# Kernel optimization log

Measured on AMD Instinct MI355X. Metric: run time of the kernel, lower is better.

The kernel has to match this reference:

```python
import jax, jax.numpy as jnp
import numpy as np

B, S, D, H, E, K = 4, 2048, 1024, 2048, 8, 2


def setup_inputs() -> dict:
    key = jax.random.key(0)
    ks = jax.random.split(key, 5)
    x = jax.random.normal(ks[0], (B, S, D), dtype=jnp.float32)
    Wr = jax.random.normal(ks[1], (D, E), dtype=jnp.float32) * 0.02  # router weight
    w1 = jax.random.normal(ks[2], (E, D, H), dtype=jnp.float32) * 0.02  # gate proj per expert
    w3 = jax.random.normal(ks[3], (E, D, H), dtype=jnp.float32) * 0.02  # up proj per expert
    w2 = jax.random.normal(ks[4], (E, H, D), dtype=jnp.float32) * 0.02  # down proj per expert
    return {"x": x, "Wr": Wr, "w1": w1, "w2": w2, "w3": w3}


def reference(x, Wr, w1, w2, w3):
    b, s, d = x.shape
    e = Wr.shape[1]
    flat = x.reshape(b * s, d)                      # [T, D]
    logits = flat @ Wr                              # [T, E]
    probs = jax.nn.softmax(logits, axis=-1)
    vals, idx = jax.lax.top_k(probs, K)             # [T, K]
    weights = vals / jnp.sum(vals, axis=-1, keepdims=True)
    onehot = jax.nn.one_hot(idx, e, dtype=flat.dtype)   # [T, K, E]
    cw = jnp.einsum('tke,tk->te', onehot, weights)      # combine weight per (token, expert)

    # naive dense: every expert computes every token, masked by combine weights
    out = jnp.zeros_like(flat)
    for ei in range(e):  # fixed small structural loop over experts
        h = jax.nn.silu(flat @ w1[ei]) * (flat @ w3[ei])   # [T, H]
        out = out + (h @ w2[ei]) * cw[:, ei:ei + 1]

    # aux load-balancing loss (usage uses any() over top-k slots, as in torch code)
    usage = (onehot.sum(axis=1) > 0).astype(flat.dtype).mean(axis=0)  # [E]
    prob_mass = probs.mean(axis=0)                                     # [E]
    aux_loss = e * jnp.sum(usage * prob_mass)
    return out.reshape(b, s, d), aux_loss
```

## Files before the change

kernel.cpp:

```cpp
#include <hip/hip_runtime.h>
#include <hip/hip_bf16.h>
#include <cstdint>
#include <cstddef>

#define T_TOK 8192
#define DIM   1024
#define HID   2048
#define NE    8
#define CAP   2816

typedef __attribute__((ext_vector_type(8))) short bf16x8;
typedef __attribute__((ext_vector_type(4))) float f32x4;
using bf16 = __hip_bfloat16;

__device__ __forceinline__ void gload16(const bf16* g, bf16* l) {
    __builtin_amdgcn_global_load_lds(
        (const __attribute__((address_space(1))) unsigned int*)(g),
        (__attribute__((address_space(3))) unsigned int*)(l), 16, 0, 0);
}
__device__ __forceinline__ float b2f(unsigned short u) {
    return __uint_as_float(((unsigned int)u) << 16);
}
#define MFMA16(a, b, c) __builtin_amdgcn_mfma_f32_16x16x32_bf16((a), (b), (c), 0, 0, 0)

__global__ __launch_bounds__(256) void k_transpose_all(const float* __restrict__ w1,
                                                       const float* __restrict__ w3,
                                                       const float* __restrict__ w2,
                                                       bf16* __restrict__ w1t,
                                                       bf16* __restrict__ w3t,
                                                       bf16* __restrict__ w2t) {
    __shared__ float tile[64][65];
    int z = blockIdx.z;
    const float* in = (z == 0) ? w1 : (z == 1) ? w3 : w2;
    bf16* out = (z == 0) ? w1t : (z == 1) ? w3t : w2t;
    int R = (z == 2) ? HID : DIM;
    int C = (z == 2) ? DIM : HID;
    int e = blockIdx.y;
    int ct = C >> 6;
    int r0 = (blockIdx.x / ct) << 6;
    int c0 = (blockIdx.x % ct) << 6;
    const float* src = in + (size_t)e * R * C;
    bf16* dst = out + (size_t)e * R * C;
    int s = threadIdx.x & 15, g = threadIdx.x >> 4;
#pragma unroll
    for (int j = 0; j < 4; ++j) {
        int row = j * 16 + g;
        float4 v = *(const float4*)(src + (size_t)(r0 + row) * C + c0 + s * 4);
        tile[row][s * 4 + 0] = v.x; tile[row][s * 4 + 1] = v.y;
        tile[row][s * 4 + 2] = v.z; tile[row][s * 4 + 3] = v.w;
    }
    __syncthreads();
#pragma unroll
    for (int j = 0; j < 4; ++j) {
        int c = j * 16 + g;
        int r = s * 4;
        bf16 o[4] = {__float2bfloat16(tile[r][c]),     __float2bfloat16(tile[r + 1][c]),
                     __float2bfloat16(tile[r + 2][c]), __float2bfloat16(tile[r + 3][c])};
        *(uint2*)(dst + (size_t)(c0 + c) * R + r0 + r) = *(const uint2*)o;
    }
}

__global__ __launch_bounds__(256) void k_logits(const float* __restrict__ x,
                                                const float* __restrict__ Wr,
                                                float* __restrict__ logits,
                                                bf16* __restrict__ xb) {
    __shared__ float wl[NE][DIM];
    for (int o = threadIdx.x; o < NE * DIM; o += 256) {
        int e = o >> 10, d = o & (DIM - 1);
        wl[e][d] = Wr[d * NE + e];
    }
    __syncthreads();
    int wid = threadIdx.x >> 6, lane = threadIdx.x & 63;
    int t = blockIdx.x * 4 + wid;
    const float* xr = x + (size_t)t * DIM;
    double acc[NE];
#pragma unroll
    for (int e = 0; e < NE; ++e) acc[e] = 0.0;
#pragma unroll
    for (int i = 0; i < DIM / 256; ++i) {
        int base = i * 256 + lane * 4;
        float4 v = *(const float4*)(xr + base);
        bf16 o[4] = {__float2bfloat16(v.x), __float2bfloat16(v.y),
                     __float2bfloat16(v.z), __float2bfloat16(v.w)};
        *(uint2*)(xb + (size_t)t * DIM + base) = *(const uint2*)o;
#pragma unroll
        for (int e = 0; e < NE; ++e)
            acc[e] += (double)v.x * wl[e][base] + (double)v.y * wl[e][base + 1]
                    + (double)v.z * wl[e][base + 2] + (double)v.w * wl[e][base + 3];
    }
#pragma unroll
    for (int e = 0; e < NE; ++e) {
        double v = acc[e];
        for (int m = 32; m >= 1; m >>= 1) v += __shfl_xor(v, m);
        if (lane == 0) logits[t * NE + e] = (float)v;
    }
}

__global__ __launch_bounds__(256) void k_route(const float* __restrict__ logits,
                                               int* counts, int* seg_tok, float* seg_w,
                                               int* slotpos, float* probsum) {
    int t = blockIdx.x * 256 + threadIdx.x;
    float l[NE];
#pragma unroll
    for (int e = 0; e < NE; ++e) l[e] = logits[t * NE + e];
    float mx = l[0];
#pragma unroll
    for (int e = 1; e < NE; ++e) mx = fmaxf(mx, l[e]);
    float p[NE], s = 0.f;
#pragma unroll
    for (int e = 0; e < NE; ++e) { p[e] = expf(l[e] - mx); s += p[e]; }
    float inv = 1.f / s;
#pragma unroll
    for (int e = 0; e < NE; ++e) p[e] *= inv;
    int e0 = 0; float v0 = p[0];
#pragma unroll
    for (int e = 1; e < NE; ++e) if (p[e] > v0) { v0 = p[e]; e0 = e; }
    int e1 = -1; float v1 = -1.f;
#pragma unroll
    for (int e = 0; e < NE; ++e) if (e != e0 && p[e] > v1) { v1 = p[e]; e1 = e; }
    float wsum = v0 + v1;
    float w0 = v0 / wsum, w1 = v1 / wsum;

    int lane = threadIdx.x & 63, wid = threadIdx.x >> 6;
    __shared__ float ps[4][NE];
#pragma unroll
    for (int e = 0; e < NE; ++e) {
        float v = p[e];
        for (int m = 32; m >= 1; m >>= 1) v += __shfl_xor(v, m);
        if (lane == 0) ps[wid][e] = v;
    }
    __syncthreads();
    if (threadIdx.x < NE) {
        float v = ps[0][threadIdx.x] + ps[1][threadIdx.x] + ps[2][threadIdx.x] + ps[3][threadIdx.x];
        atomicAdd(&probsum[threadIdx.x], v);
    }
    for (int slot = 0; slot < 2; ++slot) {
        int   e  = slot ? e1 : e0;
        float wv = slot ? w1 : w0;
#pragma unroll
        for (int ex = 0; ex < NE; ++ex) {
            unsigned long long m = __ballot(e == ex);
            if (e == ex) {
                int leader = __ffsll(m) - 1;
                int base = 0;
                if (lane == leader) base = atomicAdd(&counts[ex], __popcll(m));
                base = __shfl(base, leader);
                int pos = base + (int)__popcll(m & ((1ull << lane) - 1ull));
                if (pos < CAP) {
                    seg_tok[ex * CAP + pos] = t;
                    seg_w[ex * CAP + pos]  = wv;
                    slotpos[2 * t + slot]  = ex * CAP + pos;
                } else {
                    slotpos[2 * t + slot]  = -1;
                }
            }
        }
    }
}

__global__ __launch_bounds__(256, 3) void k_gemm1(const bf16* __restrict__ xb,
                                                  const bf16* __restrict__ w1t,
                                                  const bf16* __restrict__ w3t,
                                                  const int* __restrict__ counts,
                                                  const int* __restrict__ seg_tok,
                                                  bf16* __restrict__ h) {
    __shared__ __align__(16) bf16 lds[16384];
    __shared__ int toks[128];
    const int NTL = HID / 64;
    int flat = blockIdx.y * gridDim.x + blockIdx.x;
    int cpx  = (gridDim.x * NE) >> 3;
    int swz  = (flat & 7) * cpx + (flat >> 3);
    int e    = swz / gridDim.x;
    int tile = swz % gridDim.x;
    int mtile = tile / NTL, ntile = tile % NTL;
    int cnt = counts[e]; if (cnt > CAP) cnt = CAP;
    if (mtile * 128 >= cnt) return;

    int tx = threadIdx.x, lane = tx & 63, w = tx >> 6;
    if (tx < 128) {
        int slot = mtile * 128 + tx;
        toks[tx] = seg_tok[e * CAP + (slot < cnt ? slot : 0)];
    }
    __syncthreads();

    int l8 = lane >> 3;
    int sch = (((lane & 7) ^ l8) << 3);
    const bf16* sA[4];
#pragma unroll
    for (int i = 0; i < 4; ++i)
        sA[i] = xb + (size_t)toks[w * 32 + i * 8 + l8] * DIM + sch;
    const bf16* sBg[2];
    const bf16* sBu[2];
#pragma unroll
    for (int j = 0; j < 2; ++j) {
        int br = ntile * 64 + w * 16 + j * 8 + l8;
        sBg[j] = w1t + ((size_t)e * HID + br) * DIM + sch;
        sBu[j] = w3t + ((size_t)e * HID + br) * DIM + sch;
    }
    bf16* dA  = lds + w * 2048 + (lane << 3);
    bf16* dBg = lds + 8192  + w * 1024 + (lane << 3);
    bf16* dBu = lds + 12288 + w * 1024 + (lane << 3);

    int l15 = lane & 15, lh = lane >> 4;
    int wm = w >> 1, wn = w & 1;
    f32x4 accg[4][2], accu[4][2];
    f32x4 zero4 = {0.f, 0.f, 0.f, 0.f};
#pragma unroll
    for (int m = 0; m < 4; ++m)
#pragma unroll
        for (int n = 0; n < 2; ++n) { accg[m][n] = zero4; accu[m][n] = zero4; }

    const int NT = DIM / 64;
#pragma unroll 1
    for (int k = 0; k < NT; ++k) {
        int ko = k * 64;
#pragma unroll
        for (int i = 0; i < 4; ++i) gload16(sA[i] + ko, dA + i * 512);
#pragma unroll
        for (int j = 0; j < 2; ++j) {
            gload16(sBg[j] + ko, dBg + j * 512);
            gload16(sBu[j] + ko, dBu + j * 512);
        }
        __syncthreads();
#pragma unroll
        for (int ks = 0; ks < 2; ++ks) {
            int co = ((((ks << 2) | lh) ^ (l15 & 7)) << 3);
            bf16x8 af[4], bg[2], bu[2];
#pragma unroll
            for (int m = 0; m < 4; ++m) {
                int row = wm * 64 + m * 16 + l15;
                af[m] = *(const bf16x8*)(lds + row * 64 + co);
            }
#pragma unroll
            for (int n = 0; n < 2; ++n) {
                int br = wn * 32 + n * 16 + l15;
                bg[n] = *(const bf16x8*)(lds + 8192 + br * 64 + co);
                bu[n] = *(const bf16x8*)(lds + 12288 + br * 64 + co);
            }
#pragma unroll
            for (int n = 0; n < 2; ++n)
#pragma unroll
                for (int m = 0; m < 4; ++m) {
                    accg[m][n] = MFMA16(af[m], bg[n], accg[m][n]);
                    accu[m][n] = MFMA16(af[m], bu[n], accu[m][n]);
                }
        }
        __syncthreads();
    }

    bf16* hdst = h + ((size_t)e * CAP + (size_t)mtile * 128) * HID + ntile * 64;
#pragma unroll
    for (int m = 0; m < 4; ++m)
#pragma unroll
        for (int n = 0; n < 2; ++n)
#pragma unroll
            for (int r = 0; r < 4; ++r) {
                int row = wm * 64 + m * 16 + lh * 4 + r;
                int col = wn * 32 + n * 16 + l15;
                float gg = accg[m][n][r], uu = accu[m][n][r];
                float hv = gg / (1.f + __expf(-gg)) * uu;
                hdst[(size_t)row * HID + col] = __float2bfloat16(hv);
            }
}

__global__ __launch_bounds__(256, 3) void k_gemm2(const bf16* __restrict__ hbuf,
                                                  const bf16* __restrict__ w2t,
                                                  const int* __restrict__ counts,
                                                  const float* __restrict__ seg_w,
                                                  bf16* __restrict__ ybuf) {
    __shared__ __align__(16) bf16 lds[16384];
    __shared__ float wts[128];
    const int NTL = DIM / 128;
    int flat = blockIdx.y * gridDim.x + blockIdx.x;
    int cpx  = (gridDim.x * NE) >> 3;
    int swz  = (flat & 7) * cpx + (flat >> 3);
    int e    = swz / gridDim.x;
    int tile = swz % gridDim.x;
    int mtile = tile / NTL, ntile = tile % NTL;
    int cnt = counts[e]; if (cnt > CAP) cnt = CAP;
    if (mtile * 128 >= cnt) return;

    int tx = threadIdx.x, lane = tx & 63, w = tx >> 6;
    if (tx < 128) {
        int slot = mtile * 128 + tx;
        wts[tx] = (slot < cnt) ? seg_w[e * CAP + slot] : 0.f;
    }
    __syncthreads();

    int l8 = lane >> 3;
    int sch = (((lane & 7) ^ l8) << 3);
    const bf16* sA[4];
    const bf16* sB[4];
#pragma unroll
    for (int i = 0; i < 4; ++i) {
        sA[i] = hbuf + ((size_t)e * CAP + mtile * 128 + w * 32 + i * 8 + l8) * HID + sch;
        sB[i] = w2t + ((size_t)e * DIM + ntile * 128 + w * 32 + i * 8 + l8) * HID + sch;
    }
    bf16* dA = lds + w * 2048 + (lane << 3);
    bf16* dB = lds + 8192 + w * 2048 + (lane << 3);

    int l15 = lane & 15, lh = lane >> 4;
    int wm = w >> 1, wn = w & 1;
    f32x4 acc[4][4];
    f32x4 zero4 = {0.f, 0.f, 0.f, 0.f};
#pragma unroll
    for (int m = 0; m < 4; ++m)
#pragma unroll
        for (int n = 0; n < 4; ++n) acc[m][n] = zero4;

    const int NT = HID / 64;
#pragma unroll 1
    for (int k = 0; k < NT; ++k) {
        int ko = k * 64;
#pragma unroll
        for (int i = 0; i < 4; ++i) {
            gload16(sA[i] + ko, dA + i * 512);
            gload16(sB[i] + ko, dB + i * 512);
        }
        __syncthreads();
#pragma unroll
        for (int ks = 0; ks < 2; ++ks) {
            int co = ((((ks << 2) | lh) ^ (l15 & 7)) << 3);
            bf16x8 af[4], bf_[4];
#pragma unroll
            for (int m = 0; m < 4; ++m) {
                int row = wm * 64 + m * 16 + l15;
                af[m] = *(const bf16x8*)(lds + row * 64 + co);
                int br = wn * 64 + m * 16 + l15;
                bf_[m] = *(const bf16x8*)(lds + 8192 + br * 64 + co);
            }
#pragma unroll
            for (int n = 0; n < 4; ++n)
#pragma unroll
                for (int m = 0; m < 4; ++m)
                    acc[m][n] = MFMA16(af[m], bf_[n], acc[m][n]);
        }
        __syncthreads();
    }

    bf16* ydst = ybuf + ((size_t)e * CAP + (size_t)mtile * 128) * DIM + ntile * 128;
#pragma unroll
    for (int m = 0; m < 4; ++m)
#pragma unroll
        for (int n = 0; n < 4; ++n)
#pragma unroll
            for (int r = 0; r < 4; ++r) {
                int row = wm * 64 + m * 16 + lh * 4 + r;
                int col = wn * 64 + n * 16 + l15;
                ydst[(size_t)row * DIM + col] = __float2bfloat16(acc[m][n][r] * wts[row]);
            }
}

__global__ __launch_bounds__(256) void k_combine(const bf16* __restrict__ yb,
                                                 const int* __restrict__ slotpos,
                                                 float* __restrict__ out) {
    int t = blockIdx.x;
    int s0 = slotpos[2 * t], s1 = slotpos[2 * t + 1];
    int d = threadIdx.x * 4;
    float4 a = {0.f, 0.f, 0.f, 0.f};
    if (s0 >= 0) {
        ushort4 v = *(const ushort4*)(yb + (size_t)s0 * DIM + d);
        a.x += b2f(v.x); a.y += b2f(v.y); a.z += b2f(v.z); a.w += b2f(v.w);
    }
    if (s1 >= 0) {
        ushort4 v = *(const ushort4*)(yb + (size_t)s1 * DIM + d);
        a.x += b2f(v.x); a.y += b2f(v.y); a.z += b2f(v.z); a.w += b2f(v.w);
    }
    *(float4*)(out + (size_t)t * DIM + d) = a;
}

__global__ void k_aux(const int* __restrict__ counts, const float* __restrict__ probsum,
                      float* __restrict__ outaux) {
    if (threadIdx.x == 0 && blockIdx.x == 0) {
        float s = 0.f;
        for (int e = 0; e < NE; ++e)
            s += ((float)counts[e] / (float)T_TOK) * (probsum[e] / (float)T_TOK);
        *outaux = (float)NE * s;
    }
}

extern "C" void kernel_launch(void* const* d_in, const int* in_sizes, int n_in,
                              void* d_out, int out_size, void* d_ws, size_t ws_size,
                              hipStream_t stream) {
    const float* x  = (const float*)d_in[0];
    const float* Wr = (const float*)d_in[1];
    const float* w1 = (const float*)d_in[2];
    const float* w2 = (const float*)d_in[3];
    const float* w3 = (const float*)d_in[4];
    float* out = (float*)d_out;

    char* ws = (char*)d_ws;
    size_t off = 0;
    auto alloc = [&](size_t bytes) { void* p = ws + off; off += (bytes + 255) & ~(size_t)255; return p; };
    bf16*  xb      = (bf16*)alloc((size_t)T_TOK * DIM * 2);
    bf16*  w1t     = (bf16*)alloc((size_t)NE * HID * DIM * 2);
    bf16*  w3t     = (bf16*)alloc((size_t)NE * HID * DIM * 2);
    bf16*  w2t     = (bf16*)alloc((size_t)NE * DIM * HID * 2);
    bf16*  hbuf    = (bf16*)alloc((size_t)NE * CAP * HID * 2);
    float* logits  = (float*)alloc((size_t)T_TOK * NE * 4);
    int*   counts  = (int*)alloc(256);
    int*   segtok  = (int*)alloc((size_t)NE * CAP * 4);
    float* segw    = (float*)alloc((size_t)NE * CAP * 4);
    int*   slotpos = (int*)alloc((size_t)T_TOK * 2 * 4);
    float* probsum = (float*)alloc(256);
    bf16*  ybuf    = w1t;
    (void)ws_size; (void)in_sizes; (void)n_in;

    hipMemsetAsync(counts, 0, 256, stream);
    hipMemsetAsync(probsum, 0, 256, stream);

    k_logits<<<T_TOK / 4, 256, 0, stream>>>(x, Wr, logits, xb);
    k_route<<<T_TOK / 256, 256, 0, stream>>>(logits, counts, segtok, segw, slotpos, probsum);

    dim3 gt((DIM / 64) * (HID / 64), NE, 3);
    k_transpose_all<<<gt, 256, 0, stream>>>(w1, w3, w2, w1t, w3t, w2t);

    dim3 g1((CAP / 128) * (HID / 64), NE);
    k_gemm1<<<g1, 256, 0, stream>>>(xb, w1t, w3t, counts, segtok, hbuf);
    dim3 g2((CAP / 128) * (DIM / 128), NE);
    k_gemm2<<<g2, 256, 0, stream>>>(hbuf, w2t, counts, segw, ybuf);

    k_combine<<<T_TOK, 256, 0, stream>>>(ybuf, slotpos, out);
    k_aux<<<1, 64, 0, stream>>>(counts, probsum, out + (size_t)T_TOK * DIM);
}
```

Baseline: 387.6 us.

## Enlarge GEMM tiles to 512-thread blocks with gate/up wave roles

Both expert GEMMs move to 512-thread blocks with wider N tiles: gemm1 now covers 128 hidden columns, with half the waves computing gate and half computing up, and gemm2 covers 256 output columns. The goal is to raise reuse of the A tile in LDS and cut redundant global loads of gathered activations. In gemm1 the up-projection results pass through LDS as bf16 before the SiLU combine, which adds an extra rounding step and a sync. Fewer blocks and lower occupancy (2 blocks per CU) could hurt latency hiding.

```diff
diff --git a/kernel.cpp b/kernel.cpp
--- a/kernel.cpp
+++ b/kernel.cpp
@@ -158,15 +158,15 @@
     }
 }
 
-__global__ __launch_bounds__(256, 3) void k_gemm1(const bf16* __restrict__ xb,
+__global__ __launch_bounds__(512, 2) void k_gemm1(const bf16* __restrict__ xb,
                                                   const bf16* __restrict__ w1t,
                                                   const bf16* __restrict__ w3t,
                                                   const int* __restrict__ counts,
                                                   const int* __restrict__ seg_tok,
                                                   bf16* __restrict__ h) {
-    __shared__ __align__(16) bf16 lds[16384];
+    __shared__ __align__(16) bf16 lds[24576];
     __shared__ int toks[128];
-    const int NTL = HID / 64;
+    const int NTL = HID / 128;
     int flat = blockIdx.y * gridDim.x + blockIdx.x;
     int cpx  = (gridDim.x * NE) >> 3;
     int swz  = (flat & 7) * cpx + (flat >> 3);
@@ -185,92 +185,95 @@
 
     int l8 = lane >> 3;
     int sch = (((lane & 7) ^ l8) << 3);
-    const bf16* sA[4];
-#pragma unroll
-    for (int i = 0; i < 4; ++i)
-        sA[i] = xb + (size_t)toks[w * 32 + i * 8 + l8] * DIM + sch;
-    const bf16* sBg[2];
-    const bf16* sBu[2];
-#pragma unroll
-    for (int j = 0; j < 2; ++j) {
-        int br = ntile * 64 + w * 16 + j * 8 + l8;
-        sBg[j] = w1t + ((size_t)e * HID + br) * DIM + sch;
-        sBu[j] = w3t + ((size_t)e * HID + br) * DIM + sch;
-    }
-    bf16* dA  = lds + w * 2048 + (lane << 3);
-    bf16* dBg = lds + 8192  + w * 1024 + (lane << 3);
-    bf16* dBu = lds + 12288 + w * 1024 + (lane << 3);
+    const bf16* sp[6];
+    bf16* dp[6];
+#pragma unroll
+    for (int i = 0; i < 6; ++i) {
+        int c = w * 6 + i;
+        dp[i] = lds + c * 512 + (lane << 3);
+        if (c < 16)
+            sp[i] = xb + (size_t)toks[c * 8 + l8] * DIM + sch;
+        else if (c < 32)
+            sp[i] = w1t + ((size_t)e * HID + ntile * 128 + (c - 16) * 8 + l8) * DIM + sch;
+        else
+            sp[i] = w3t + ((size_t)e * HID + ntile * 128 + (c - 32) * 8 + l8) * DIM + sch;
+    }
 
     int l15 = lane & 15, lh = lane >> 4;
-    int wm = w >> 1, wn = w & 1;
-    f32x4 accg[4][2], accu[4][2];
+    int role = w >> 2, rh = (w >> 1) & 1, ch = w & 1;
+    const int bbase = 8192 + role * 8192;
+    f32x4 acc[4][4];
     f32x4 zero4 = {0.f, 0.f, 0.f, 0.f};
 #pragma unroll
     for (int m = 0; m < 4; ++m)
 #pragma unroll
-        for (int n = 0; n < 2; ++n) { accg[m][n] = zero4; accu[m][n] = zero4; }
+        for (int n = 0; n < 4; ++n) acc[m][n] = zero4;
 
     const int NT = DIM / 64;
 #pragma unroll 1
     for (int k = 0; k < NT; ++k) {
         int ko = k * 64;
 #pragma unroll
-        for (int i = 0; i < 4; ++i) gload16(sA[i] + ko, dA + i * 512);
-#pragma unroll
-        for (int j = 0; j < 2; ++j) {
-            gload16(sBg[j] + ko, dBg + j * 512);
-            gload16(sBu[j] + ko, dBu + j * 512);
+        for (int i = 0; i < 6; ++i) gload16(sp[i] + ko, dp[i]);
+        __syncthreads();
+#pragma unroll
+        for (int ks = 0; ks < 2; ++ks) {
+            int co = ((((ks << 2) | lh) ^ (l15 & 7)) << 3);
+            bf16x8 af[4], bb[4];
+#pragma unroll
+            for (int m = 0; m < 4; ++m)
+                af[m] = *(const bf16x8*)(lds + (rh * 64 + m * 16 + l15) * 64 + co);
+#pragma unroll
+            for (int n = 0; n < 4; ++n)
+                bb[n] = *(const bf16x8*)(lds + bbase + (ch * 64 + n * 16 + l15) * 64 + co);
+#pragma unroll
+            for (int n = 0; n < 4; ++n)
+#pragma unroll
+                for (int m = 0; m < 4; ++m)
+                    acc[m][n] = MFMA16(af[m], bb[n], acc[m][n]);
         }
         __syncthreads();
-#pragma unroll
-        for (int ks = 0; ks < 2; ++ks) {
-            int co = ((((ks << 2) | lh) ^ (l15 & 7)) << 3);
-            bf16x8 af[4], bg[2], bu[2];
-#pragma unroll
-            for (int m = 0; m < 4; ++m) {
-                int row = wm * 64 + m * 16 + l15;
-                af[m] = *(const bf16x8*)(lds + row * 64 + co);
-            }
-#pragma unroll
-            for (int n = 0; n < 2; ++n) {
-                int br = wn * 32 + n * 16 + l15;
-                bg[n] = *(const bf16x8*)(lds + 8192 + br * 64 + co);
-                bu[n] = *(const bf16x8*)(lds + 12288 + br * 64 + co);
-            }
-#pragma unroll
-            for (int n = 0; n < 2; ++n)
-#pragma unroll
-                for (int m = 0; m < 4; ++m) {
-                    accg[m][n] = MFMA16(af[m], bg[n], accg[m][n]);
-                    accu[m][n] = MFMA16(af[m], bu[n], accu[m][n]);
+    }
+
+    if (role == 1) {
+#pragma unroll
+        for (int m = 0; m < 4; ++m)
+#pragma unroll
+            for (int n = 0; n < 4; ++n)
+#pragma unroll
+                for (int r = 0; r < 4; ++r) {
+                    int row = rh * 64 + m * 16 + lh * 4 + r;
+                    int col = ch * 64 + n * 16 + l15;
+                    lds[row * 128 + col] = __float2bfloat16(acc[m][n][r]);
                 }
-        }
-        __syncthreads();
-    }
-
-    bf16* hdst = h + ((size_t)e * CAP + (size_t)mtile * 128) * HID + ntile * 64;
-#pragma unroll
-    for (int m = 0; m < 4; ++m)
-#pragma unroll
-        for (int n = 0; n < 2; ++n)
-#pragma unroll
-            for (int r = 0; r < 4; ++r) {
-                int row = wm * 64 + m * 16 + lh * 4 + r;
-                int col = wn * 32 + n * 16 + l15;
-                float gg = accg[m][n][r], uu = accu[m][n][r];
-                float hv = gg / (1.f + __expf(-gg)) * uu;
-                hdst[(size_t)row * HID + col] = __float2bfloat16(hv);
-            }
-}
-
-__global__ __launch_bounds__(256, 3) void k_gemm2(const bf16* __restrict__ hbuf,
+    }
+    __syncthreads();
+    if (role == 0) {
+        bf16* hdst = h + ((size_t)e * CAP + (size_t)mtile * 128) * HID + ntile * 128;
+#pragma unroll
+        for (int m = 0; m < 4; ++m)
+#pragma unroll
+            for (int n = 0; n < 4; ++n)
+#pragma unroll
+                for (int r = 0; r < 4; ++r) {
+                    int row = rh * 64 + m * 16 + lh * 4 + r;
+                    int col = ch * 64 + n * 16 + l15;
+                    float gg = acc[m][n][r];
+                    float uu = b2f(*(const unsigned short*)&lds[row * 128 + col]);
+                    float hv = gg / (1.f + __expf(-gg)) * uu;
+                    hdst[(size_t)row * HID + col] = __float2bfloat16(hv);
+                }
+    }
+}
+
+__global__ __launch_bounds__(512, 2) void k_gemm2(const bf16* __restrict__ hbuf,
                                                   const bf16* __restrict__ w2t,
                                                   const int* __restrict__ counts,
                                                   const float* __restrict__ seg_w,
                                                   bf16* __restrict__ ybuf) {
-    __shared__ __align__(16) bf16 lds[16384];
+    __shared__ __align__(16) bf16 lds[24576];
     __shared__ float wts[128];
-    const int NTL = DIM / 128;
+    const int NTL = DIM / 256;
     int flat = blockIdx.y * gridDim.x + blockIdx.x;
     int cpx  = (gridDim.x * NE) >> 3;
     int swz  = (flat & 7) * cpx + (flat >> 3);
@@ -289,18 +292,20 @@
 
     int l8 = lane >> 3;
     int sch = (((lane & 7) ^ l8) << 3);
-    const bf16* sA[4];
-    const bf16* sB[4];
-#pragma unroll
-    for (int i = 0; i < 4; ++i) {
-        sA[i] = hbuf + ((size_t)e * CAP + mtile * 128 + w * 32 + i * 8 + l8) * HID + sch;
-        sB[i] = w2t + ((size_t)e * DIM + ntile * 128 + w * 32 + i * 8 + l8) * HID + sch;
-    }
-    bf16* dA = lds + w * 2048 + (lane << 3);
-    bf16* dB = lds + 8192 + w * 2048 + (lane << 3);
+    const bf16* sp[6];
+    bf16* dp[6];
+#pragma unroll
+    for (int i = 0; i < 6; ++i) {
+        int c = w * 6 + i;
+        dp[i] = lds + c * 512 + (lane << 3);
+        if (c < 16)
+            sp[i] = hbuf + ((size_t)e * CAP + mtile * 128 + c * 8 + l8) * HID + sch;
+        else
+            sp[i] = w2t + ((size_t)e * DIM + ntile * 256 + (c - 16) * 8 + l8) * HID + sch;
+    }
 
     int l15 = lane & 15, lh = lane >> 4;
-    int wm = w >> 1, wn = w & 1;
+    int wm = w >> 2, wn = w & 3;
     f32x4 acc[4][4];
     f32x4 zero4 = {0.f, 0.f, 0.f, 0.f};
 #pragma unroll
@@ -313,32 +318,28 @@
     for (int k = 0; k < NT; ++k) {
         int ko = k * 64;
 #pragma unroll
-        for (int i = 0; i < 4; ++i) {
-            gload16(sA[i] + ko, dA + i * 512);
-            gload16(sB[i] + ko, dB + i * 512);
+        for (int i = 0; i < 6; ++i) gload16(sp[i] + ko, dp[i]);
+        __syncthreads();
+#pragma unroll
+        for (int ks = 0; ks < 2; ++ks) {
+            int co = ((((ks << 2) | lh) ^ (l15 & 7)) << 3);
+            bf16x8 af[4], bb[4];
+#pragma unroll
+            for (int m = 0; m < 4; ++m)
+                af[m] = *(const bf16x8*)(lds + (wm * 64 + m * 16 + l15) * 64 + co);
+#pragma unroll
+            for (int n = 0; n < 4; ++n)
+                bb[n] = *(const bf16x8*)(lds + 8192 + (wn * 64 + n * 16 + l15) * 64 + co);
+#pragma unroll
+            for (int n = 0; n < 4; ++n)
+#pragma unroll
+                for (int m = 0; m < 4; ++m)
+                    acc[m][n] = MFMA16(af[m], bb[n], acc[m][n]);
         }
         __syncthreads();
-#pragma unroll
-        for (int ks = 0; ks < 2; ++ks) {
-            int co = ((((ks << 2) | lh) ^ (l15 & 7)) << 3);
-            bf16x8 af[4], bf_[4];
-#pragma unroll
-            for (int m = 0; m < 4; ++m) {
-                int row = wm * 64 + m * 16 + l15;
-                af[m] = *(const bf16x8*)(lds + row * 64 + co);
-                int br = wn * 64 + m * 16 + l15;
-                bf_[m] = *(const bf16x8*)(lds + 8192 + br * 64 + co);
-            }
-#pragma unroll
-            for (int n = 0; n < 4; ++n)
-#pragma unroll
-                for (int m = 0; m < 4; ++m)
-                    acc[m][n] = MFMA16(af[m], bf_[n], acc[m][n]);
-        }
-        __syncthreads();
-    }
-
-    bf16* ydst = ybuf + ((size_t)e * CAP + (size_t)mtile * 128) * DIM + ntile * 128;
+    }
+
+    bf16* ydst = ybuf + ((size_t)e * CAP + (size_t)mtile * 128) * DIM + ntile * 256;
 #pragma unroll
     for (int m = 0; m < 4; ++m)
 #pragma unroll
@@ -415,10 +416,10 @@
     dim3 gt((DIM / 64) * (HID / 64), NE, 3);
     k_transpose_all<<<gt, 256, 0, stream>>>(w1, w3, w2, w1t, w3t, w2t);
 
-    dim3 g1((CAP / 128) * (HID / 64), NE);
-    k_gemm1<<<g1, 256, 0, stream>>>(xb, w1t, w3t, counts, segtok, hbuf);
-    dim3 g2((CAP / 128) * (DIM / 128), NE);
-    k_gemm2<<<g2, 256, 0, stream>>>(hbuf, w2t, counts, segw, ybuf);
+    dim3 g1((CAP / 128) * (HID / 128), NE);
+    k_gemm1<<<g1, 512, 0, stream>>>(xb, w1t, w3t, counts, segtok, hbuf);
+    dim3 g2((CAP / 128) * (DIM / 256), NE);
+    k_gemm2<<<g2, 512, 0, stream>>>(hbuf, w2t, counts, segw, ybuf);
 
     k_combine<<<T_TOK, 256, 0, stream>>>(ybuf, slotpos, out);
     k_aux<<<1, 64, 0, stream>>>(counts, probsum, out + (size_t)T_TOK * DIM);
```

Measured after the change: 391.3 us. About the same (+1.0%).
